# Optimization experiments

Measured on AMD Instinct MI355X. Metric: run time of the kernel, lower is better.

The kernel has to match this reference:

```python
import math
import jax, jax.numpy as jnp
import numpy as np

B, T, E = 2, 2048, 1024
H, KV = 16, 4
D = E // H          # 64
G = H // KV         # 4 groups


def rotate_half(x):
    x1, x2 = jnp.split(x, 2, axis=-1)
    return jnp.concatenate([-x2, x1], axis=-1)


def setup_inputs() -> dict:
    key = jax.random.key(0)
    ks = jax.random.split(key, 12)
    query = jax.random.normal(ks[0], (B, T, E), jnp.float32)
    key_t = jax.random.normal(ks[1], (B, T, E), jnp.float32)
    value = jax.random.normal(ks[2], (B, T, E), jnp.float32)
    # RoPE tables: [T, D]
    inv_freq = 1.0 / (10000.0 ** (np.arange(0, D, 2, dtype=np.float32) / D))
    pos = np.arange(T, dtype=np.float32)
    freqs = np.outer(pos, inv_freq)                      # [T, D/2]
    emb = np.concatenate([freqs, freqs], axis=-1)        # [T, D]
    cos_emb = jnp.asarray(np.cos(emb), jnp.float32)
    sin_emb = jnp.asarray(np.sin(emb), jnp.float32)
    # causal mask [1,1,T,T], True = keep
    mask = jnp.tril(jnp.ones((T, T), bool))[None, None, :, :]
    s = 0.02
    Wq = jax.random.normal(ks[3], (E, H * D), jnp.float32) * s
    bq = jnp.zeros((H * D,), jnp.float32)
    Wk = jax.random.normal(ks[4], (E, KV * D), jnp.float32) * s
    bk = jnp.zeros((KV * D,), jnp.float32)
    Wv = jax.random.normal(ks[5], (E, KV * D), jnp.float32) * s
    bv = jnp.zeros((KV * D,), jnp.float32)
    Wo = jax.random.normal(ks[6], (E, E), jnp.float32) * s
    bo = jnp.zeros((E,), jnp.float32)
    return {"query": query, "key": key_t, "value": value,
            "cos_emb": cos_emb, "sin_emb": sin_emb, "mask": mask,
            "Wq": Wq, "bq": bq, "Wk": Wk, "bk": bk,
            "Wv": Wv, "bv": bv, "Wo": Wo, "bo": bo}


def reference(query, key, value, cos_emb, sin_emb, mask,
              Wq, bq, Wk, bk, Wv, bv, Wo, bo):
    Bq, Tq, _ = query.shape
    Tk = key.shape[1]
    q = (query @ Wq + bq).reshape(Bq, Tq, H, D)          # [B,Tq,H,D]
    k = (key @ Wk + bk).reshape(Bq, Tk, KV, D)           # [B,Tk,KV,D]
    v = (value @ Wv + bv).reshape(Bq, Tk, KV, D)
    # expand kv heads across groups (head h = kv*G + g, consecutive repeat)
    k = jnp.repeat(k, G, axis=2)                         # [B,Tk,H,D]
    v = jnp.repeat(v, G, axis=2)
    # RoPE (applied post-expansion, as in the original)
    cos = cos_emb[None, :, None, :]                      # [1,T,1,D]
    sin = sin_emb[None, :, None, :]
    q = q * cos[:, :Tq] + rotate_half(q) * sin[:, :Tq]
    k = k * cos[:, :Tk] + rotate_half(k) * sin[:, :Tk]
    scores = jnp.einsum('bqhd,bkhd->bhqk', q, k) / math.sqrt(D)
    scores = jnp.where(mask[:, :, :Tq, :Tk], scores, jnp.float32(-jnp.inf))
    probs = jax.nn.softmax(scores, axis=-1)              # [B,H,Tq,Tk]
    attn = jnp.einsum('bhqk,bkhd->bqhd', probs, v).reshape(Bq, Tq, E)
    return attn @ Wo + bo
```

## Files before the change

### kernel.cpp

```cpp
#include <hip/hip_runtime.h>
#include <hip/hip_bf16.h>

constexpr int Bc  = 2;
constexpr int Tc  = 2048;
constexpr int Ec  = 1024;
constexpr int Hc  = 16;
constexpr int KVc = 4;
constexpr int Dc  = 64;

typedef short bf16x8 __attribute__((ext_vector_type(8)));
typedef short short4v __attribute__((ext_vector_type(4)));
typedef float f32x4  __attribute__((ext_vector_type(4)));
typedef float f32x16 __attribute__((ext_vector_type(16)));
typedef int   i32x4  __attribute__((ext_vector_type(4)));

__device__ inline short f2bf_bits(float f) {
    union { __hip_bfloat16 h; short s; } u;
    u.h = __float2bfloat16(f);
    return u.s;
}

__device__ inline float bf2f(short s) {
    union { short s16; __hip_bfloat16 h; } u;
    u.s16 = s;
    return __bfloat162float(u.h);
}

__device__ inline unsigned pkbf(float a, float b) {
    return (unsigned)(unsigned short)f2bf_bits(a)
         | ((unsigned)(unsigned short)f2bf_bits(b) << 16);
}

__device__ inline float fexp2(float x) { return __builtin_exp2f(x); }

__device__ inline void gload16(const short* g, short* lds) {
    __builtin_amdgcn_global_load_lds(
        (const __attribute__((address_space(1))) unsigned int*)g,
        (__attribute__((address_space(3))) unsigned int*)lds,
        16, 0, 0);
}

__global__ __launch_bounds__(256) void conv3_f32_bf16(
    const float* __restrict__ q, const float* __restrict__ k,
    const float* __restrict__ v,
    short* __restrict__ Xq, short* __restrict__ Xk, short* __restrict__ Xv)
{
    const int range = blockIdx.x >> 12;
    const int sub   = blockIdx.x & 4095;
    const float* x = range == 0 ? q : (range == 1 ? k : v);
    short*       y = range == 0 ? Xq : (range == 1 ? Xk : Xv);
    int i = (sub * 256 + threadIdx.x) * 4;
    float4 vv = *reinterpret_cast<const float4*>(x + i);
    short4v o;
    o[0] = f2bf_bits(vv.x);
    o[1] = f2bf_bits(vv.y);
    o[2] = f2bf_bits(vv.z);
    o[3] = f2bf_bits(vv.w);
    *reinterpret_cast<short4v*>(y + i) = o;
}

__global__ __launch_bounds__(256) void transp_all(
    const float* __restrict__ Wq, const float* __restrict__ Wk,
    const float* __restrict__ Wv, const float* __restrict__ Wo,
    short* __restrict__ Wqt, short* __restrict__ Wkt,
    short* __restrict__ Wvt, short* __restrict__ Wot)
{
    __shared__ float tile[32][33];
    const int id = blockIdx.x;
    const float* W; short* Wt; int N, bx, by;
    if (id < 1024)      { W = Wq; Wt = Wqt; N = 1024; bx = id & 31;          by = id >> 5; }
    else if (id < 1280) { W = Wk; Wt = Wkt; N = 256;  bx = (id - 1024) & 7;  by = (id - 1024) >> 3; }
    else if (id < 1536) { W = Wv; Wt = Wvt; N = 256;  bx = (id - 1280) & 7;  by = (id - 1280) >> 3; }
    else                { W = Wo; Wt = Wot; N = 1024; bx = (id - 1536) & 31; by = (id - 1536) >> 5; }
    const int K = 1024;
    int nb = bx * 32, kb = by * 32;
    int tx = threadIdx.x & 31, ty = threadIdx.x >> 5;
    #pragma unroll
    for (int j = 0; j < 4; ++j)
        tile[ty + j * 8][tx] = W[(size_t)(kb + ty + j * 8) * N + nb + tx];
    __syncthreads();
    #pragma unroll
    for (int j = 0; j < 4; ++j)
        Wt[(size_t)(nb + ty + j * 8) * K + kb + tx] = f2bf_bits(tile[tx][ty + j * 8]);
}

#define GEMM_CORE(A_, Bt_, Kdim_)                                              \
    const int lane = threadIdx.x & 63;                                         \
    const int w    = threadIdx.x >> 6;                                         \
    const int wm   = w >> 1, wn = w & 1;                                       \
    const int rin  = lane >> 3;                                                \
    const int swc  = ((lane & 7) ^ rin) * 8;                                   \
    f32x4 acc[4][2] = {};                                                      \
    for (int k0 = 0; k0 < (Kdim_); k0 += 64) {                                 \
        _Pragma("unroll")                                                      \
        for (int i2 = 0; i2 < 4; ++i2) {                                       \
            const int r = w * 32 + i2 * 8;                                     \
            gload16((A_) + (size_t)(m0 + r + rin) * (Kdim_) + k0 + swc,        \
                    As + r * 64);                                              \
        }                                                                      \
        _Pragma("unroll")                                                      \
        for (int i2 = 0; i2 < 2; ++i2) {                                       \
            const int r = w * 16 + i2 * 8;                                     \
            gload16((Bt_) + (size_t)(n0 + r + rin) * (Kdim_) + k0 + swc,       \
                    Bs + r * 64);                                              \
        }                                                                      \
        __syncthreads();                                                       \
        _Pragma("unroll")                                                      \
        for (int ks = 0; ks < 2; ++ks) {                                       \
            bf16x8 af[4], bfr[2];                                              \
            _Pragma("unroll")                                                  \
            for (int mi = 0; mi < 4; ++mi) {                                   \
                int row = wm * 64 + mi * 16 + (lane & 15);                     \
                int sl  = (ks * 4 + (lane >> 4)) ^ (row & 7);                  \
                af[mi] = *reinterpret_cast<const bf16x8*>(As + row * 64 + sl * 8); \
            }                                                                  \
            _Pragma("unroll")                                                  \
            for (int ni = 0; ni < 2; ++ni) {                                   \
                int row = wn * 32 + ni * 16 + (lane & 15);                     \
                int sl  = (ks * 4 + (lane >> 4)) ^ (row & 7);                  \
                bfr[ni] = *reinterpret_cast<const bf16x8*>(Bs + row * 64 + sl * 8); \
            }                                                                  \
            _Pragma("unroll")                                                  \
            for (int mi = 0; mi < 4; ++mi)                                     \
                _Pragma("unroll")                                              \
                for (int ni = 0; ni < 2; ++ni)                                 \
                    acc[mi][ni] = __builtin_amdgcn_mfma_f32_16x16x32_bf16(     \
                        af[mi], bfr[ni], acc[mi][ni], 0, 0, 0);                \
        }                                                                      \
        __syncthreads();                                                       \
    }

__global__ __launch_bounds__(256) void gemm_qkv(
    const short* __restrict__ Xq, const short* __restrict__ Xk,
    const short* __restrict__ Xv,
    const short* __restrict__ Wqt, const short* __restrict__ Wkt,
    const short* __restrict__ Wvt,
    const float* __restrict__ bq, const float* __restrict__ bk,
    const float* __restrict__ bv,
    short* __restrict__ Qp, short* __restrict__ Kp, short* __restrict__ VTp)
{
    __shared__ short As[128 * 64];
    __shared__ short Bs[64 * 64];
    const int gid = blockIdx.x;
    const short *A, *Bt; const float* bias; int bx, by, mode;
    if (gid < 512)      { mode = 0; A = Xq; Bt = Wqt; bias = bq; bx = gid & 15;         by = gid >> 4; }
    else if (gid < 640) { mode = 1; A = Xk; Bt = Wkt; bias = bk; bx = (gid - 512) & 3;  by = (gid - 512) >> 2; }
    else                { mode = 2; A = Xv; Bt = Wvt; bias = bv; bx = (gid - 640) & 3;  by = (gid - 640) >> 2; }
    const int m0 = by * 128, n0 = bx * 64;

    GEMM_CORE(A, Bt, 1024)

    #pragma unroll
    for (int mi = 0; mi < 4; ++mi)
        #pragma unroll
        for (int ni = 0; ni < 2; ++ni) {
            int col = n0 + wn * 32 + ni * 16 + (lane & 15);
            float bv2 = bias[col];
            #pragma unroll
            for (int i = 0; i < 4; ++i) {
                int row = m0 + wm * 64 + mi * 16 + ((lane >> 4) * 4) + i;
                float v = acc[mi][ni][i] + bv2;
                if (mode == 0)
                    Qp[(size_t)row * 1024 + col] = f2bf_bits(v);
                else if (mode == 1)
                    Kp[(size_t)row * 256 + col] = f2bf_bits(v);
                else
                    VTp[(((size_t)(row >> 11) * 256 + col) << 11) + (row & 2047)]
                        = f2bf_bits(v);
            }
        }
}

__global__ __launch_bounds__(256) void gemm_o(
    const short* __restrict__ A, const short* __restrict__ Bt,
    const float* __restrict__ bias, float* __restrict__ C)
{
    __shared__ short As[128 * 64];
    __shared__ short Bs[64 * 64];
    const int m0 = blockIdx.y * 128, n0 = blockIdx.x * 64;

    GEMM_CORE(A, Bt, 1024)

    #pragma unroll
    for (int mi = 0; mi < 4; ++mi)
        #pragma unroll
        for (int ni = 0; ni < 2; ++ni) {
            int col = n0 + wn * 32 + ni * 16 + (lane & 15);
            float bv2 = bias[col];
            #pragma unroll
            for (int i = 0; i < 4; ++i) {
                int row = m0 + wm * 64 + mi * 16 + ((lane >> 4) * 4) + i;
                C[(size_t)row * 1024 + col] = acc[mi][ni][i] + bv2;
            }
        }
}

__global__ __launch_bounds__(256) void rope_merged(
    short* __restrict__ Qp, short* __restrict__ Kp,
    const float* __restrict__ cosE, const float* __restrict__ sinE)
{
    short* x; int hbits; float scale; int idx;
    if (blockIdx.x < 2048) {
        x = Qp; hbits = 4; scale = 0.125f * 1.44269504089f;
        idx = blockIdx.x * 256 + threadIdx.x;
    } else {
        x = Kp; hbits = 2; scale = 1.0f;
        idx = (blockIdx.x - 2048) * 256 + threadIdx.x;
    }
    int dq  = (idx & 7) * 4;
    int hh  = (idx >> 3) & ((1 << hbits) - 1);
    int row = idx >> (3 + hbits);
    int t   = row & (Tc - 1);
    float4 c4 = *reinterpret_cast<const float4*>(cosE + t * 64 + dq);
    float4 s4 = *reinterpret_cast<const float4*>(sinE + t * 64 + dq);
    size_t base = (size_t)row * (64 << hbits) + hh * 64 + dq;
    short4v a = *reinterpret_cast<const short4v*>(x + base);
    short4v b = *reinterpret_cast<const short4v*>(x + base + 32);
    short4v oa, ob;
    float c[4] = {c4.x, c4.y, c4.z, c4.w};
    float s[4] = {s4.x, s4.y, s4.z, s4.w};
    #pragma unroll
    for (int j = 0; j < 4; ++j) {
        float x1 = bf2f(a[j]), x2 = bf2f(b[j]);
        oa[j] = f2bf_bits((x1 * c[j] - x2 * s[j]) * scale);
        ob[j] = f2bf_bits((x2 * c[j] + x1 * s[j]) * scale);
    }
    *reinterpret_cast<short4v*>(x + base)      = oa;
    *reinterpret_cast<short4v*>(x + base + 32) = ob;
}

__global__ __launch_bounds__(256, 4) void flash_gqa4(
    const short* __restrict__ Q,
    const short* __restrict__ Kx,
    const short* __restrict__ VT,
    short* __restrict__ attn,
    short* __restrict__ PO,
    float* __restrict__ ML)
{
    __shared__ short smem[16384];

    const int lane = threadIdx.x & 63;
    const int w    = threadIdx.x >> 6;
    const int lo   = lane & 31;
    const int hi   = lane >> 5;

    const int L   = blockIdx.x;
    const int xcd = L & 7;
    const int j   = L >> 3;
    const int g   = j & 3;
    const int u   = 39 - (j >> 2);
    int qt = 0, rem = u;
    while (true) { int nc0 = (qt >> 2) + 1; if (rem < nc0) break; rem -= nc0; ++qt; }
    const int c  = rem;
    const int nc = (qt >> 2) + 1;
    const int b   = xcd >> 2;
    const int kvh = xcd & 3;
    const int h   = kvh * 4 + g;
    const int slot = (b * 16 + h) * 40 + u;

    const int q0w = qt * 128 + w * 32;
    const int qg  = q0w + lo;

    bf16x8 qf[4];
    {
        const short* qp = Q + (size_t)(b * Tc + qg) * Ec + h * 64 + hi * 8;
        #pragma unroll
        for (int ds = 0; ds < 4; ++ds)
            qf[ds] = *reinterpret_cast<const bf16x8*>(qp + 16 * ds);
    }
    const short* Kb = Kx + (size_t)b * Tc * (KVc * Dc) + kvh * 64;
    const short* Vb = VT + (size_t)(b * KVc + kvh) * 64 * Tc;

    const int rin = lane >> 3;
    const int swc = ((lane & 7) ^ rin) * 8;
    auto stage = [&](int bufi, int kb2) {
        #pragma unroll
        for (int i2 = 0; i2 < 2; ++i2) {
            const int row = w * 16 + i2 * 8;
            gload16(Kb + (size_t)(kb2 + row + rin) * 256 + swc,
                    smem + bufi * 4096 + row * 64);
            gload16(Vb + (size_t)(row + rin) * Tc + kb2 + swc,
                    smem + 8192 + bufi * 4096 + row * 64);
        }
    };

    const int t0 = c * 8;
    const int t1 = min(c * 8 + 8, 2 * qt + 2);
    stage(0, t0 * 64);

    float m = -1e30f, l = 0.f;
    f32x16 o0 = {}, o1 = {};
    const int kv_hi = q0w + 32;

    for (int t = t0; t < t1; ++t) {
        const int kb  = t * 64;
        const int cur = (t - t0) & 1;
        if (t + 1 < t1) {
            stage(cur ^ 1, kb + 64);
            asm volatile("s_waitcnt vmcnt(4)" ::: "memory");
        } else {
            asm volatile("s_waitcnt vmcnt(0)" ::: "memory");
        }
        __builtin_amdgcn_s_barrier();

        if (kb < kv_hi) {
            const short* Kl = smem + cur * 4096;
            const short* Vl = smem + 8192 + cur * 4096;
            bf16x8 kf[2][4], vf[2][4];
            #pragma unroll
            for (int t2 = 0; t2 < 2; ++t2)
                #pragma unroll
                for (int ds = 0; ds < 4; ++ds) {
                    int row = 32 * t2 + lo;
                    int sl  = (2 * ds + hi) ^ (lo & 7);
                    kf[t2][ds] = *reinterpret_cast<const bf16x8*>(Kl + row * 64 + sl * 8);
                }
            #pragma unroll
            for (int td = 0; td < 2; ++td)
                #pragma unroll
                for (int sl2 = 0; sl2 < 4; ++sl2) {
                    int row = 32 * td + lo;
                    int sl  = (2 * sl2 + hi) ^ (lo & 7);
                    vf[td][sl2] = *reinterpret_cast<const bf16x8*>(Vl + row * 64 + sl * 8);
                }

            f32x16 s0 = {}, s1 = {};
            #pragma unroll
            for (int ds = 0; ds < 4; ++ds) {
                s0 = __builtin_amdgcn_mfma_f32_32x32x16_bf16(kf[0][ds], qf[ds], s0, 0, 0, 0);
                s1 = __builtin_amdgcn_mfma_f32_32x32x16_bf16(kf[1][ds], qf[ds], s1, 0, 0, 0);
            }

            if (kb + 63 > q0w) {
                #pragma unroll
                for (int r = 0; r < 16; ++r) {
                    int kkl = (r & 3) + 8 * (r >> 2) + 4 * hi;
                    if (kb + kkl > qg)      s0[r] = -1e30f;
                    if (kb + 32 + kkl > qg) s1[r] = -1e30f;
                }
            }

            float mx[8];
            #pragma unroll
            for (int j2 = 0; j2 < 8; ++j2)
                mx[j2] = fmaxf(fmaxf(s0[2 * j2], s0[2 * j2 + 1]),
                               fmaxf(s1[2 * j2], s1[2 * j2 + 1]));
            #pragma unroll
            for (int st = 4; st > 0; st >>= 1)
                #pragma unroll
                for (int j2 = 0; j2 < st; ++j2) mx[j2] = fmaxf(mx[j2], mx[j2 + st]);
            float pm = fmaxf(mx[0], __shfl_xor(mx[0], 32));

            float corr = 1.0f;
            if (__any(pm > m + 8.0f)) {
                float mn = fmaxf(m, pm);
                corr = fexp2(m - mn);
                m = mn;
                #pragma unroll
                for (int r = 0; r < 16; ++r) { o0[r] *= corr; o1[r] *= corr; }
            }
            float rs = 0.f;
            #pragma unroll
            for (int r = 0; r < 16; ++r) {
                s0[r] = fexp2(s0[r] - m);
                s1[r] = fexp2(s1[r] - m);
                rs += s0[r] + s1[r];
            }
            rs += __shfl_xor(rs, 32);
            l = l * corr + rs;

            #pragma unroll
            for (int t2 = 0; t2 < 2; ++t2) {
                f32x16 sv = t2 ? s1 : s0;
                unsigned wv[8], sx[8];
                #pragma unroll
                for (int j2 = 0; j2 < 8; ++j2) wv[j2] = pkbf(sv[2 * j2], sv[2 * j2 + 1]);
                #pragma unroll
                for (int j2 = 0; j2 < 8; ++j2) sx[j2] = __shfl_xor(wv[j2], 32);
                #pragma unroll
                for (int u2 = 0; u2 < 2; ++u2) {
                    union { unsigned u4[4]; bf16x8 v; } pf;
                    pf.u4[0] = hi ? sx[4 * u2 + 2] : wv[4 * u2];
                    pf.u4[1] = hi ? sx[4 * u2 + 3] : wv[4 * u2 + 1];
                    pf.u4[2] = hi ? wv[4 * u2 + 2] : sx[4 * u2];
                    pf.u4[3] = hi ? wv[4 * u2 + 3] : sx[4 * u2 + 1];
                    int sl = 2 * t2 + u2;
                    o0 = __builtin_amdgcn_mfma_f32_32x32x16_bf16(vf[0][sl], pf.v, o0, 0, 0, 0);
                    o1 = __builtin_amdgcn_mfma_f32_32x32x16_bf16(vf[1][sl], pf.v, o1, 0, 0, 0);
                }
            }
        }
        __builtin_amdgcn_s_barrier();
    }

    const float inv = (nc == 1) ? (1.0f / l) : 1.0f;
    short* ob = smem + w * 2048;
    #pragma unroll
    for (int r = 0; r < 16; ++r) {
        int d0 = (r & 3) + 8 * (r >> 2) + 4 * hi;
        ob[lo * 64 + ( d0       ^ ((lo & 7) << 3))] = f2bf_bits(o0[r] * inv);
        ob[lo * 64 + ((d0 + 32) ^ ((lo & 7) << 3))] = f2bf_bits(o1[r] * inv);
    }
    if (nc > 1 && hi == 0) {
        ML[(size_t)slot * 256 + (w * 32 + lo) * 2]     = m;
        ML[(size_t)slot * 256 + (w * 32 + lo) * 2 + 1] = l;
    }
    #pragma unroll
    for (int j2 = 0; j2 < 4; ++j2) {
        int row = lane >> 1;
        int c8  = ((lane & 1) * 4 + j2) * 8;
        bf16x8 v = *reinterpret_cast<const bf16x8*>(
            ob + row * 64 + (c8 ^ ((row & 7) << 3)));
        if (nc == 1)
            *reinterpret_cast<bf16x8*>(
                attn + (size_t)(b * Tc + q0w + row) * Ec + h * 64 + c8) = v;
        else
            *reinterpret_cast<bf16x8*>(
                PO + (size_t)slot * 8192 + (w * 32 + row) * 64 + c8) = v;
    }
}

__global__ __launch_bounds__(256) void combine_kernel(
    const short* __restrict__ PO, const float* __restrict__ ML,
    short* __restrict__ attn)
{
    const int qt    = 4 + (blockIdx.x >> 2);
    const int rg    = blockIdx.x & 3;
    const int combo = blockIdx.y;
    const int h = combo & 15, b = combo >> 4;
    const int nc = (qt >> 2) + 1;
    const int k  = qt >> 2, r4 = qt & 3;
    const int base = (k + 1) * (2 * k + r4);
    const int slot0 = combo * 40 + base;

    const int r  = rg * 32 + (threadIdx.x >> 3);
    const int d8 = (threadIdx.x & 7) * 8;

    float mv[4], lv[4];
    float M = -1e30f;
    #pragma unroll 4
    for (int cc = 0; cc < nc; ++cc) {
        mv[cc] = ML[(size_t)(slot0 + cc) * 256 + r * 2];
        lv[cc] = ML[(size_t)(slot0 + cc) * 256 + r * 2 + 1];
        M = fmaxf(M, mv[cc]);
    }
    float Lsum = 0.f;
    float a[8] = {};
    #pragma unroll 4
    for (int cc = 0; cc < nc; ++cc) {
        float wgt = fexp2(mv[cc] - M);
        Lsum += wgt * lv[cc];
        bf16x8 po = *reinterpret_cast<const bf16x8*>(
            PO + (size_t)(slot0 + cc) * 8192 + r * 64 + d8);
        #pragma unroll
        for (int j = 0; j < 8; ++j) a[j] += wgt * bf2f(po[j]);
    }
    float inv = 1.0f / Lsum;
    bf16x8 o;
    #pragma unroll
    for (int j = 0; j < 8; ++j) o[j] = f2bf_bits(a[j] * inv);
    *reinterpret_cast<bf16x8*>(
        attn + (size_t)(b * Tc + qt * 128 + r) * Ec + h * 64 + d8) = o;
}

extern "C" void kernel_launch(void* const* d_in, const int* in_sizes, int n_in,
                              void* d_out, int out_size, void* d_ws, size_t ws_size,
                              hipStream_t stream)
{
    const float* query = (const float*)d_in[0];
    const float* key   = (const float*)d_in[1];
    const float* value = (const float*)d_in[2];
    const float* cosE  = (const float*)d_in[3];
    const float* sinE  = (const float*)d_in[4];
    const float* Wq = (const float*)d_in[6];
    const float* bq = (const float*)d_in[7];
    const float* Wk = (const float*)d_in[8];
    const float* bk = (const float*)d_in[9];
    const float* Wv = (const float*)d_in[10];
    const float* bv = (const float*)d_in[11];
    const float* Wo = (const float*)d_in[12];
    const float* bo = (const float*)d_in[13];

    char* ws = (char*)d_ws;
    constexpr size_t MB = 1u << 20;
    short* Xq   = (short*)(ws + 0);
    short* Xk   = (short*)(ws + 8  * MB);
    short* Xv   = (short*)(ws + 16 * MB);
    short* Wqt  = (short*)(ws + 24 * MB);
    short* Wkt  = (short*)(ws + 26 * MB);
    short* Wvt  = (short*)(ws + 26 * MB + 512 * 1024);
    short* Wot  = (short*)(ws + 27 * MB);
    short* Qp   = (short*)(ws + 29 * MB);
    short* Kp   = (short*)(ws + 37 * MB);
    short* VTp  = (short*)(ws + 39 * MB);
    short* attn = (short*)(ws + 41 * MB);
    short* PO   = (short*)(ws + 0);
    float* ML   = (float*)(ws + 21 * MB);
    (void)ws_size;

    conv3_f32_bf16<<<12288, 256, 0, stream>>>(query, key, value, Xq, Xk, Xv);
    transp_all<<<2560, 256, 0, stream>>>(Wq, Wk, Wv, Wo, Wqt, Wkt, Wvt, Wot);
    gemm_qkv<<<768, 256, 0, stream>>>(Xq, Xk, Xv, Wqt, Wkt, Wvt,
                                      bq, bk, bv, Qp, Kp, VTp);
    rope_merged<<<2560, 256, 0, stream>>>(Qp, Kp, cosE, sinE);
    flash_gqa4<<<1280, 256, 0, stream>>>(Qp, Kp, VTp, attn, PO, ML);
    combine_kernel<<<dim3(48, 32), 256, 0, stream>>>(PO, ML, attn);
    gemm_o<<<dim3(16, 32), 256, 0, stream>>>(attn, Wot, bo, (float*)d_out);
}
```

Before: 134.5 us.

## Restructure flash attention loop to use one barrier with interleaved LDS loads

The flash-attention main loop now waits for the current tile, takes a single barrier, and only then prefetches the next K/V tile. This removes the second per-iteration barrier. K and V fragments are read from LDS right next to the MFMAs that use them, instead of all being preloaded into registers, which lowers register pressure. The MFMA sections are wrapped in s_setprio, and the packed bf16 conversion uses the paired intrinsic. Launch bounds drop from 4 to 3 blocks per SIMD, which allows more registers per thread but can reduce occupancy. The prefetch is now issued later in each iteration, so load latency may be less hidden.

```diff
diff --git a/kernel.cpp b/kernel.cpp
--- a/kernel.cpp
+++ b/kernel.cpp
@@ -27,8 +27,9 @@
 }
 
 __device__ inline unsigned pkbf(float a, float b) {
-    return (unsigned)(unsigned short)f2bf_bits(a)
-         | ((unsigned)(unsigned short)f2bf_bits(b) << 16);
+    union { __hip_bfloat162 h2; unsigned u; } u;
+    u.h2 = __float22bfloat162_rn(float2{a, b});
+    return u.u;
 }
 
 __device__ inline float fexp2(float x) { return __builtin_exp2f(x); }
@@ -229,7 +230,7 @@
     *reinterpret_cast<short4v*>(x + base + 32) = ob;
 }
 
-__global__ __launch_bounds__(256, 4) void flash_gqa4(
+__global__ __launch_bounds__(256, 3) void flash_gqa6(
     const short* __restrict__ Q,
     const short* __restrict__ Kx,
     const short* __restrict__ VT,
@@ -284,6 +285,11 @@
         }
     };
 
+    int slot8[4];
+    #pragma unroll
+    for (int i = 0; i < 4; ++i)
+        slot8[i] = (((2 * i + hi) ^ (lo & 7)) * 8) + lo * 64;
+
     const int t0 = c * 8;
     const int t1 = min(c * 8 + 8, 2 * qt + 2);
     stage(0, t0 * 64);
@@ -295,41 +301,24 @@
     for (int t = t0; t < t1; ++t) {
         const int kb  = t * 64;
         const int cur = (t - t0) & 1;
-        if (t + 1 < t1) {
-            stage(cur ^ 1, kb + 64);
-            asm volatile("s_waitcnt vmcnt(4)" ::: "memory");
-        } else {
-            asm volatile("s_waitcnt vmcnt(0)" ::: "memory");
-        }
+        asm volatile("s_waitcnt vmcnt(0)" ::: "memory");
         __builtin_amdgcn_s_barrier();
+        if (t + 1 < t1) stage(cur ^ 1, kb + 64);
 
         if (kb < kv_hi) {
             const short* Kl = smem + cur * 4096;
-            const short* Vl = smem + 8192 + cur * 4096;
-            bf16x8 kf[2][4], vf[2][4];
-            #pragma unroll
-            for (int t2 = 0; t2 < 2; ++t2)
-                #pragma unroll
-                for (int ds = 0; ds < 4; ++ds) {
-                    int row = 32 * t2 + lo;
-                    int sl  = (2 * ds + hi) ^ (lo & 7);
-                    kf[t2][ds] = *reinterpret_cast<const bf16x8*>(Kl + row * 64 + sl * 8);
-                }
-            #pragma unroll
-            for (int td = 0; td < 2; ++td)
-                #pragma unroll
-                for (int sl2 = 0; sl2 < 4; ++sl2) {
-                    int row = 32 * td + lo;
-                    int sl  = (2 * sl2 + hi) ^ (lo & 7);
-                    vf[td][sl2] = *reinterpret_cast<const bf16x8*>(Vl + row * 64 + sl * 8);
-                }
+            const short* Vl = Kl + 8192;
 
             f32x16 s0 = {}, s1 = {};
+            __builtin_amdgcn_s_setprio(1);
             #pragma unroll
             for (int ds = 0; ds < 4; ++ds) {
-                s0 = __builtin_amdgcn_mfma_f32_32x32x16_bf16(kf[0][ds], qf[ds], s0, 0, 0, 0);
-                s1 = __builtin_amdgcn_mfma_f32_32x32x16_bf16(kf[1][ds], qf[ds], s1, 0, 0, 0);
-            }
+                bf16x8 k0 = *reinterpret_cast<const bf16x8*>(Kl + slot8[ds]);
+                bf16x8 k1 = *reinterpret_cast<const bf16x8*>(Kl + slot8[ds] + 2048);
+                s0 = __builtin_amdgcn_mfma_f32_32x32x16_bf16(k0, qf[ds], s0, 0, 0, 0);
+                s1 = __builtin_amdgcn_mfma_f32_32x32x16_bf16(k1, qf[ds], s1, 0, 0, 0);
+            }
+            __builtin_amdgcn_s_setprio(0);
 
             if (kb + 63 > q0w) {
                 #pragma unroll
@@ -371,27 +360,31 @@
 
             #pragma unroll
             for (int t2 = 0; t2 < 2; ++t2) {
-                f32x16 sv = t2 ? s1 : s0;
-                unsigned wv[8], sx[8];
+                const f32x16& sv = t2 ? s1 : s0;
+                unsigned pw[8], sx[8];
                 #pragma unroll
-                for (int j2 = 0; j2 < 8; ++j2) wv[j2] = pkbf(sv[2 * j2], sv[2 * j2 + 1]);
+                for (int j2 = 0; j2 < 8; ++j2) pw[j2] = pkbf(sv[2 * j2], sv[2 * j2 + 1]);
                 #pragma unroll
-                for (int j2 = 0; j2 < 8; ++j2) sx[j2] = __shfl_xor(wv[j2], 32);
+                for (int j2 = 0; j2 < 8; ++j2) sx[j2] = __shfl_xor(pw[j2], 32);
                 #pragma unroll
                 for (int u2 = 0; u2 < 2; ++u2) {
                     union { unsigned u4[4]; bf16x8 v; } pf;
-                    pf.u4[0] = hi ? sx[4 * u2 + 2] : wv[4 * u2];
-                    pf.u4[1] = hi ? sx[4 * u2 + 3] : wv[4 * u2 + 1];
-                    pf.u4[2] = hi ? wv[4 * u2 + 2] : sx[4 * u2];
-                    pf.u4[3] = hi ? wv[4 * u2 + 3] : sx[4 * u2 + 1];
+                    pf.u4[0] = hi ? sx[4 * u2 + 2] : pw[4 * u2];
+                    pf.u4[1] = hi ? sx[4 * u2 + 3] : pw[4 * u2 + 1];
+                    pf.u4[2] = hi ? pw[4 * u2 + 2] : sx[4 * u2];
+                    pf.u4[3] = hi ? pw[4 * u2 + 3] : sx[4 * u2 + 1];
                     int sl = 2 * t2 + u2;
-                    o0 = __builtin_amdgcn_mfma_f32_32x32x16_bf16(vf[0][sl], pf.v, o0, 0, 0, 0);
-                    o1 = __builtin_amdgcn_mfma_f32_32x32x16_bf16(vf[1][sl], pf.v, o1, 0, 0, 0);
+                    bf16x8 v0 = *reinterpret_cast<const bf16x8*>(Vl + slot8[sl]);
+                    bf16x8 v1 = *reinterpret_cast<const bf16x8*>(Vl + slot8[sl] + 2048);
+                    __builtin_amdgcn_s_setprio(1);
+                    o0 = __builtin_amdgcn_mfma_f32_32x32x16_bf16(v0, pf.v, o0, 0, 0, 0);
+                    o1 = __builtin_amdgcn_mfma_f32_32x32x16_bf16(v1, pf.v, o1, 0, 0, 0);
+                    __builtin_amdgcn_s_setprio(0);
                 }
             }
         }
-        __builtin_amdgcn_s_barrier();
-    }
+    }
+    __builtin_amdgcn_s_barrier();
 
     const float inv = (nc == 1) ? (1.0f / l) : 1.0f;
     short* ob = smem + w * 2048;
@@ -503,7 +496,7 @@
     gemm_qkv<<<768, 256, 0, stream>>>(Xq, Xk, Xv, Wqt, Wkt, Wvt,
                                       bq, bk, bv, Qp, Kp, VTp);
     rope_merged<<<2560, 256, 0, stream>>>(Qp, Kp, cosE, sinE);
-    flash_gqa4<<<1280, 256, 0, stream>>>(Qp, Kp, VTp, attn, PO, ML);
+    flash_gqa6<<<1280, 256, 0, stream>>>(Qp, Kp, VTp, attn, PO, ML);
     combine_kernel<<<dim3(48, 32), 256, 0, stream>>>(PO, ML, attn);
     gemm_o<<<dim3(16, 32), 256, 0, stream>>>(attn, Wot, bo, (float*)d_out);
 }
```

New measurement: 120.3 us. -10.5%, faster.
